# Kernel optimization log

Measured on AMD Instinct MI355X. Metric: run time of the kernel, lower is better.

## Reference

```python
import jax, jax.numpy as jnp
import numpy as np

B, T, NS, NP, F, FO, K1, K2 = 128, 24, 20, 8, 256, 256, 3, 2
ES_EXTRA, EP_EXTRA = 60, 16


def _edges(n, n_extra, seed):
    # ring in both directions guarantees every node has in- and out-degree >= 1
    rng = np.random.default_rng(seed)
    i = np.arange(n)
    src = np.concatenate([i, (i + 1) % n, rng.integers(0, n, n_extra)])
    dst = np.concatenate([(i + 1) % n, i, rng.integers(0, n, n_extra)])
    return jnp.asarray(np.stack([src, dst]).astype(np.int32))


def _dconv(X, row, col, ew, W, b):
    # X: [B, N, Cin], W: [2, K, Cin, Cout]  (torch_geometric_temporal DConv)
    N = X.shape[1]
    deg_out = jnp.zeros((N,), X.dtype).at[row].add(ew)
    deg_in = jnp.zeros((N,), X.dtype).at[col].add(ew)
    norm_out = (1.0 / deg_out)[row]
    norm_in = (1.0 / deg_in)[row]

    def prop(x, norm):
        msg = x[:, row, :] * norm[None, :, None]  # gather at source, scale
        return jnp.zeros_like(x).at[:, col, :].add(msg)  # scatter-add at target

    H = X @ W[0, 0] + X @ W[1, 0]
    K = W.shape[1]
    Tx_0 = X
    if K > 1:
        Tx_1_o = prop(X, norm_out)
        Tx_1_i = prop(X, norm_in)
        H = H + Tx_1_o @ W[0, 1] + Tx_1_i @ W[1, 1]
        for k in range(2, K):
            Tx_2_o = 2.0 * prop(Tx_1_o, norm_out) - Tx_0
            Tx_2_i = 2.0 * prop(Tx_1_i, norm_in) - Tx_0
            H = H + Tx_2_o @ W[0, k] + Tx_2_i @ W[1, k]
            Tx_0, Tx_1_o, Tx_1_i = Tx_1_o, Tx_2_o, Tx_2_i
    return H + b


def _forward(x_dis, x_precip, edge_index_s, edge_weight_s, edge_index_p, edge_weight_p,
             Wz_s, bz_s, Wz_p, bz_p, Wr_s, br_s, Wr_p, br_p, Wh_s, bh_s, Wh_p, bh_p,
             W_ro, b_ro, W_ag, b_ag):
    b_, t_, ns, _ = x_dis.shape
    np_ = x_precip.shape[2]
    fo = Wz_s.shape[-1]
    rs, cs = edge_index_s[0], edge_index_s[1]
    rp, cp = edge_index_p[0], edge_index_p[1]

    def gate(Xs, Xp, Hs, Hp, Ws, bs, Wp, bp):
        Gs = _dconv(jnp.concatenate([Xs, Hs], axis=-1), rs, cs, edge_weight_s, Ws, bs)
        Gp = _dconv(jnp.concatenate([Xp, Hp], axis=-1), rp, cp, edge_weight_p, Wp, bp)
        return jnp.concatenate([Gs, Gp], axis=1)

    def step(H, xt):
        Xs, Xp = xt
        Hs, Hp = H[:, :ns], H[:, ns:]
        Z = jax.nn.sigmoid(gate(Xs, Xp, Hs, Hp, Wz_s, bz_s, Wz_p, bz_p))
        R = jax.nn.sigmoid(gate(Xs, Xp, Hs, Hp, Wr_s, br_s, Wr_p, br_p))
        gH = H * R
        Ht = jnp.tanh(gate(Xs, Xp, gH[:, :ns], gH[:, ns:], Wh_s, bh_s, Wh_p, bh_p))
        return Z * H + (1.0 - Z) * Ht, None

    H0 = jnp.zeros((b_, ns + np_, fo), x_dis.dtype)
    H, _ = jax.lax.scan(step, H0, (jnp.swapaxes(x_dis, 0, 1), jnp.swapaxes(x_precip, 0, 1)))
    out = H @ W_ro + b_ro                       # [B, 28, 1] readout per node
    out = (out[:, :, 0] @ W_ag + b_ag)[:, :, None]  # aggr over 28 nodes -> [B, 5, 1]
    return out


def setup_inputs() -> dict:
    key = jax.random.key(0)
    ks = jax.random.split(key, 24)
    sc = 0.04  # ~1/sqrt(fan_in=512)
    d = {
        'x_dis': jax.random.normal(ks[0], (B, T, NS, F), jnp.float32),
        'x_precip': jax.random.normal(ks[1], (B, T, NP, F), jnp.float32),
        'edge_index_s': _edges(NS, ES_EXTRA, 1),
        'edge_index_p': _edges(NP, EP_EXTRA, 2),
        'edge_weight_s': jax.random.uniform(ks[2], (2 * NS + ES_EXTRA,), jnp.float32, 0.1, 1.0),
        'edge_weight_p': jax.random.uniform(ks[3], (2 * NP + EP_EXTRA,), jnp.float32, 0.1, 1.0),
    }
    names_s = ['Wz_s', 'Wr_s', 'Wh_s']
    names_p = ['Wz_p', 'Wr_p', 'Wh_p']
    for i, n in enumerate(names_s):
        d[n] = sc * jax.random.normal(ks[4 + i], (2, K1, F + FO, FO), jnp.float32)
        d['b' + n[1:]] = sc * jax.random.normal(ks[7 + i], (FO,), jnp.float32)
    for i, n in enumerate(names_p):
        d[n] = sc * jax.random.normal(ks[10 + i], (2, K2, F + FO, FO), jnp.float32)
        d['b' + n[1:]] = sc * jax.random.normal(ks[13 + i], (FO,), jnp.float32)
    d['W_ro'] = sc * jax.random.normal(ks[16], (FO, 1), jnp.float32)
    d['b_ro'] = sc * jax.random.normal(ks[17], (1,), jnp.float32)
    d['W_ag'] = 0.1 * jax.random.normal(ks[18], (NS + NP, 5), jnp.float32)
    d['b_ag'] = 0.1 * jax.random.normal(ks[19], (5,), jnp.float32)
    return d


def reference(x_dis, x_precip, edge_index_s, edge_weight_s, edge_index_p, edge_weight_p,
              Wz_s, bz_s, Wz_p, bz_p, Wr_s, br_s, Wr_p, br_p, Wh_s, bh_s, Wh_p, bh_p,
              W_ro, b_ro, W_ag, b_ag):
    return _forward(x_dis, x_precip, edge_index_s, edge_weight_s, edge_index_p, edge_weight_p,
                    Wz_s, bz_s, Wz_p, bz_p, Wr_s, br_s, Wr_p, br_p, Wh_s, bh_s, Wh_p, bh_p,
                    W_ro, b_ro, W_ag, b_ag)
```

## Files before the change

### kernel.cpp

```cpp
#include <hip/hip_runtime.h>
#include <stdint.h>

#define NSN 20
#define NPN 8
#define NB 128
#define TT 24
#define NN 28
#define ES 100
#define EP 32
#define KHS 1280
#define KHP 768
#define NPRE 768
#define TCH 4

typedef _Float16 half_t;
typedef __attribute__((ext_vector_type(8))) _Float16 f16x8;
typedef __attribute__((ext_vector_type(4))) float f32x4;

__device__ __forceinline__ void gl16(const half_t* g, half_t* l) {
  __builtin_amdgcn_global_load_lds((const __attribute__((address_space(1))) void*)g,
                                   (__attribute__((address_space(3))) void*)l, 16, 0, 0);
}

__global__ void graph_build(const int* __restrict__ ei_s, const float* __restrict__ ew_s,
                            const int* __restrict__ ei_p, const float* __restrict__ ew_p,
                            float* __restrict__ Ms_s, float* __restrict__ Ms_p,
                            float* __restrict__ Mbig_s, float* __restrict__ Mbig_p) {
  __shared__ float Ao[NSN*NSN], Aiw[NSN*NSN], dgo[NSN], dgi[NSN];
  __shared__ float T2o[NSN*NSN], T2i[NSN*NSN];
  __shared__ float Aop[NPN*NPN], Aip[NPN*NPN], dgop[NPN], dgip[NPN];
  int tid = threadIdx.x;
  for (int i = tid; i < NSN*NSN; i += blockDim.x) { Ao[i] = 0.f; Aiw[i] = 0.f; }
  for (int i = tid; i < NPN*NPN; i += blockDim.x) { Aop[i] = 0.f; Aip[i] = 0.f; }
  if (tid < NSN) { dgo[tid] = 0.f; dgi[tid] = 0.f; }
  if (tid < NPN) { dgop[tid] = 0.f; dgip[tid] = 0.f; }
  __syncthreads();
  if (tid == 0) {
    for (int e = 0; e < ES; ++e) { int r = ei_s[e], c = ei_s[ES+e]; float w = ew_s[e]; dgo[r] += w; dgi[c] += w; }
    for (int e = 0; e < ES; ++e) { int r = ei_s[e], c = ei_s[ES+e]; Ao[c*NSN+r] += 1.f/dgo[r]; Aiw[c*NSN+r] += 1.f/dgi[r]; }
  }
  if (tid == 1) {
    for (int e = 0; e < EP; ++e) { int r = ei_p[e], c = ei_p[EP+e]; float w = ew_p[e]; dgop[r] += w; dgip[c] += w; }
    for (int e = 0; e < EP; ++e) { int r = ei_p[e], c = ei_p[EP+e]; Aop[c*NPN+r] += 1.f/dgop[r]; Aip[c*NPN+r] += 1.f/dgip[r]; }
  }
  __syncthreads();
  for (int i = tid; i < NSN*NSN; i += blockDim.x) {
    int r = i / NSN, c = i % NSN;
    float so = 0.f, si = 0.f;
    for (int k = 0; k < NSN; ++k) { so += Ao[r*NSN+k]*Ao[k*NSN+c]; si += Aiw[r*NSN+k]*Aiw[k*NSN+c]; }
    float t2o = 2.f*so - (r==c ? 1.f : 0.f);
    float t2i = 2.f*si - (r==c ? 1.f : 0.f);
    T2o[i] = t2o; T2i[i] = t2i;
    Ms_s[0*NSN*NSN + i] = Ao[i];
    Ms_s[1*NSN*NSN + i] = Aiw[i];
    Ms_s[2*NSN*NSN + i] = t2o;
    Ms_s[3*NSN*NSN + i] = t2i;
  }
  for (int i = tid; i < NPN*NPN; i += blockDim.x) {
    Ms_p[0*NPN*NPN + i] = Aop[i];
    Ms_p[1*NPN*NPN + i] = Aip[i];
  }
  __syncthreads();
  for (int i = tid; i < NSN*NSN*5; i += blockDim.x) {
    int n = i / 100, s = i % 100, r = s / 5, tau = s % 5;
    float v;
    if (tau == 0) v = (n == r) ? 1.f : 0.f;
    else if (tau == 1) v = Ao[n*NSN + r];
    else if (tau == 2) v = Aiw[n*NSN + r];
    else if (tau == 3) v = T2o[n*NSN + r];
    else               v = T2i[n*NSN + r];
    Mbig_s[i] = v;
  }
  for (int i = tid; i < NPN*NPN*3; i += blockDim.x) {
    int n = i / 24, s = i % 24, r = s / 3, tau = s % 3;
    float v;
    if (tau == 0) v = (n == r) ? 1.f : 0.f;
    else if (tau == 1) v = Aop[n*NPN + r];
    else               v = Aip[n*NPN + r];
    Mbig_p[i] = v;
  }
}

__device__ __forceinline__ float wsrc(const float* W, int Kdim, int tau, int i, int jj) {
  if (tau == 0) return W[(size_t)(0*Kdim+0)*512*256 + (size_t)i*256 + jj]
                     + W[(size_t)(1*Kdim+0)*512*256 + (size_t)i*256 + jj];
  int dir = (tau - 1) & 1;
  int k = (tau + 1) >> 1;
  return W[(size_t)(dir*Kdim + k)*512*256 + (size_t)i*256 + jj];
}

__global__ void prep_w(const float* __restrict__ Wz_s, const float* __restrict__ Wr_s, const float* __restrict__ Wh_s,
                       const float* __restrict__ Wz_p, const float* __restrict__ Wr_p, const float* __restrict__ Wh_p,
                       half_t* __restrict__ WX_s, half_t* __restrict__ WX_p,
                       half_t* __restrict__ WHzr_s, half_t* __restrict__ WHh_s,
                       half_t* __restrict__ WHzr_p, half_t* __restrict__ WHh_p) {
  const long c0 = (long)768*KHS;
  const long c1 = c0 + (long)768*KHP;
  const long c2 = c1 + (long)2560*256;
  const long c3 = c2 + (long)1280*256;
  const long c4 = c3 + (long)1536*256;
  const long c5 = c4 + (long)768*256;
  for (long idx = (long)blockIdx.x*256 + threadIdx.x; idx < c5; idx += (long)gridDim.x*256) {
    if (idx < c0) {
      long x = idx; int j = (int)(x / KHS), c = (int)(x % KHS); int tau = c >> 8;
      const float* W = (j < 256) ? Wz_s : (j < 512) ? Wr_s : Wh_s;
      WX_s[x] = (half_t)wsrc(W, 3, tau, c & 255, j & 255);
    } else if (idx < c1) {
      long x = idx - c0; int j = (int)(x / KHP), c = (int)(x % KHP); int tau = c >> 8;
      const float* W = (j < 256) ? Wz_p : (j < 512) ? Wr_p : Wh_p;
      WX_p[x] = (half_t)wsrc(W, 2, tau, c & 255, j & 255);
    } else if (idx < c2) {
      long x = idx - c1; int cc = (int)(x >> 8), f = (int)(x & 255);
      int tau = cc / 512, j = cc % 512;
      const float* W = (j < 256) ? Wz_s : Wr_s;
      WHzr_s[(size_t)cc*256 + f] = (half_t)wsrc(W, 3, tau, 256 + f, j & 255);
    } else if (idx < c3) {
      long x = idx - c2; int cc = (int)(x >> 8), f = (int)(x & 255);
      int tau = cc >> 8, j = cc & 255;
      WHh_s[(size_t)cc*256 + f] = (half_t)wsrc(Wh_s, 3, tau, 256 + f, j);
    } else if (idx < c4) {
      long x = idx - c3; int cc = (int)(x >> 8), f = (int)(x & 255);
      int tau = cc / 512, j = cc % 512;
      const float* W = (j < 256) ? Wz_p : Wr_p;
      WHzr_p[(size_t)cc*256 + f] = (half_t)wsrc(W, 2, tau, 256 + f, j & 255);
    } else {
      long x = idx - c4; int cc = (int)(x >> 8), f = (int)(x & 255);
      int tau = cc >> 8, j = cc & 255;
      WHh_p[(size_t)cc*256 + f] = (half_t)wsrc(Wh_p, 2, tau, 256 + f, j);
    }
  }
}

__global__ void zero_f(float* p, long n) {
  long i = (long)blockIdx.x*256 + threadIdx.x;
  if (i < n) p[i] = 0.f;
}

__global__ __launch_bounds__(256) void chebx(const float* __restrict__ xdis, const float* __restrict__ xpre,
                                             const float* __restrict__ Ms_s, const float* __restrict__ Ms_p,
                                             half_t* __restrict__ XTs, half_t* __restrict__ XTp, int t0) {
  __shared__ float Xc[NSN*256];
  __shared__ float Ml[4*NSN*NSN];
  int bb = blockIdx.x, tid = threadIdx.x;
  bool isP = bb >= NB*TCH;
  int q = isP ? bb - NB*TCH : bb;
  int b = q % NB, tp = q / NB;
  int N = isP ? NPN : NSN, nt = isP ? 3 : 5, KX = nt << 8;
  const float* X = isP ? (xpre + (size_t)(b*TT + t0 + tp)*NPN*256)
                       : (xdis + (size_t)(b*TT + t0 + tp)*NSN*256);
  for (int i = tid; i < N*64; i += 256) ((float4*)Xc)[i] = ((const float4*)X)[i];
  int nm = (nt-1)*N*N;
  const float* Msrc = isP ? Ms_p : Ms_s;
  for (int i = tid; i < nm; i += 256) Ml[i] = Msrc[i];
  __syncthreads();
  half_t* XT = isP ? XTp : XTs;
  size_t rowbase = (size_t)(tp*NB + b)*N;
  int kc8 = KX >> 3, nch = N * kc8;
  for (int i = tid; i < nch; i += 256) {
    int n = i / kc8, c8 = i - n*kc8;
    int tau = c8 >> 5, f0 = (c8 & 31) << 3;
    float v[8];
    if (tau == 0) {
      const float* xr0 = Xc + n*256 + f0;
#pragma unroll
      for (int j = 0; j < 8; ++j) v[j] = xr0[j];
    } else {
      const float* M = Ml + (tau-1)*N*N + n*N;
#pragma unroll
      for (int j = 0; j < 8; ++j) v[j] = 0.f;
      for (int r = 0; r < N; ++r) {
        float m = M[r];
        const float* xr = Xc + r*256 + f0;
#pragma unroll
        for (int j = 0; j < 8; ++j) v[j] += m*xr[j];
      }
    }
    union { uint4 q; half_t u[8]; } hv;
#pragma unroll
    for (int j = 0; j < 8; ++j) hv.u[j] = (half_t)v[j];
    *(uint4*)(XT + (rowbase + n)*(size_t)KX + ((size_t)c8 << 3)) = hv.q;
  }
}

__global__ __launch_bounds__(512) void gemm_pre(
    const half_t* __restrict__ A0, const half_t* __restrict__ B0, int K0,
    int rbS, int cbTot,
    const half_t* __restrict__ A1, const half_t* __restrict__ B1, int K1,
    half_t* __restrict__ Px0, half_t* __restrict__ Px1,
    const float* __restrict__ bz0, const float* __restrict__ br0, const float* __restrict__ bh0,
    const float* __restrict__ bz1, const float* __restrict__ br1, const float* __restrict__ bh1) {
  __shared__ __align__(16) half_t sbuf[3][12288];
  int id = blockIdx.x;
  int xx = id & 7, kq = id >> 3;
  int rbTot8 = (gridDim.x / cbTot) >> 3;
  int rb = xx*rbTot8 + kq / cbTot;
  int cb = kq - (kq / cbTot)*cbTot;

  bool isP = rb >= rbS;
  const half_t* A = isP ? A1 : A0;
  const half_t* B = isP ? B1 : B0;
  int K = isP ? K1 : K0;
  int row0 = (isP ? rb - rbS : rb) * 64;
  int col0 = cb * 128;
  int tid = threadIdx.x, lane = tid & 63, w = tid >> 6;
  int l15 = lane & 15, l4 = lane >> 4;
  int wr = (w >> 2) * 32, wc = (w & 3) * 32;

  const half_t* srcb[3];
  int ldso[3];
#pragma unroll
  for (int j = 0; j < 3; ++j) {
    int c = ((j*8 + w) << 6) + lane;
    const half_t* base;
    if (c < 512) {
      int r = c >> 3, kb = c & 7;
      base = A + (size_t)(row0 + r)*K + ((kb ^ (r & 7)) << 3);
    } else {
      int d = c - 512, r = d >> 3, kb = d & 7;
      base = B + (size_t)(col0 + r)*K + ((kb ^ (r & 7)) << 3);
    }
    srcb[j] = base;
    ldso[j] = c << 3;
  }

  f32x4 acc[2][2];
#pragma unroll
  for (int i = 0; i < 2; ++i)
#pragma unroll
    for (int j = 0; j < 2; ++j) acc[i][j] = (f32x4){0.f,0.f,0.f,0.f};

  int nk = K >> 6;
#define STAGEP(K0E, BUFP)  { half_t* _b = (BUFP); _Pragma("unroll") \
    for (int j = 0; j < 3; ++j) gl16(srcb[j] + (K0E), _b + ldso[j]); }

  STAGEP(0,   &sbuf[0][0]);
  STAGEP(64,  &sbuf[1][0]);
  STAGEP(128, &sbuf[2][0]);

  for (int k = 0; k < nk; ++k) {
    int rem = nk - 1 - k;
    if (rem >= 2)      asm volatile("s_waitcnt vmcnt(6)" ::: "memory");
    else if (rem == 1) asm volatile("s_waitcnt vmcnt(3)" ::: "memory");
    else               asm volatile("s_waitcnt vmcnt(0)" ::: "memory");
    __builtin_amdgcn_s_barrier();
    const half_t* cur = &sbuf[k % 3][0];
    const half_t* cB = cur + 4096;
#pragma unroll
    for (int kk = 0; kk < 2; ++kk) {
      f16x8 af[2], bq[2];
#pragma unroll
      for (int mi = 0; mi < 2; ++mi) {
        int r = wr + mi*16 + l15;
        int sb = (kk*4 + l4) ^ (r & 7);
        af[mi] = *(const f16x8*)&cur[r*64 + sb*8];
      }
#pragma unroll
      for (int ni = 0; ni < 2; ++ni) {
        int r = wc + ni*16 + l15;
        int sb = (kk*4 + l4) ^ (r & 7);
        bq[ni] = *(const f16x8*)&cB[r*64 + sb*8];
      }
#pragma unroll
      for (int mi = 0; mi < 2; ++mi)
#pragma unroll
        for (int ni = 0; ni < 2; ++ni)
          acc[mi][ni] = __builtin_amdgcn_mfma_f32_16x16x32_f16(af[mi], bq[ni], acc[mi][ni], 0, 0, 0);
    }
    __builtin_amdgcn_s_barrier();
    if (k + 3 < nk) STAGEP((k + 3) << 6, &sbuf[k % 3][0]);
  }
#undef STAGEP

  half_t* PxO = isP ? Px1 : Px0;
#pragma unroll
  for (int mi = 0; mi < 2; ++mi)
#pragma unroll
    for (int ni = 0; ni < 2; ++ni) {
      int colg = col0 + wc + ni*16 + l15;
      const float* bias = (colg < 256) ? (isP ? bz1 : bz0)
                        : (colg < 512) ? (isP ? br1 : br0)
                                       : (isP ? bh1 : bh0);
#pragma unroll
      for (int rg = 0; rg < 4; ++rg) {
        int grow = row0 + wr + mi*16 + l4*4 + rg;
        PxO[(size_t)grow*NPRE + colg] = (half_t)(acc[mi][ni][rg] + bias[colg & 255]);
      }
    }
}

__global__ __launch_bounds__(512) void gemm_y(
    const half_t* __restrict__ A0, const half_t* __restrict__ B0, half_t* __restrict__ C0, int NC0, int cb0, int nb0,
    const half_t* __restrict__ A1, const half_t* __restrict__ B1, half_t* __restrict__ C1, int NC1, int cb1) {
  __shared__ __align__(16) half_t sbuf[3][12288];
  int id = blockIdx.x;
  int rb, cb; const half_t *A, *B; half_t* C; int NC;
  if (id < nb0) { rb = id / cb0; cb = id % cb0; A = A0; B = B0; C = C0; NC = NC0; }
  else { int q = id - nb0; rb = q / cb1; cb = q % cb1; A = A1; B = B1; C = C1; NC = NC1; }
  int row0 = rb*64, col0 = cb*128;
  int tid = threadIdx.x, lane = tid & 63, w = tid >> 6;
  int l15 = lane & 15, l4 = lane >> 4;
  int wr = (w >> 2) * 32, wc = (w & 3) * 32;

  const half_t* srcb[3];
  int ldso[3];
#pragma unroll
  for (int j = 0; j < 3; ++j) {
    int c = ((j*8 + w) << 6) + lane;
    const half_t* base;
    if (c < 512) {
      int r = c >> 3, kb = c & 7;
      base = A + (size_t)(row0 + r)*256 + ((kb ^ (r & 7)) << 3);
    } else {
      int d = c - 512, r = d >> 3, kb = d & 7;
      base = B + (size_t)(col0 + r)*256 + ((kb ^ (r & 7)) << 3);
    }
    srcb[j] = base;
    ldso[j] = c << 3;
  }

  f32x4 acc[2][2];
#pragma unroll
  for (int i = 0; i < 2; ++i)
#pragma unroll
    for (int j = 0; j < 2; ++j) acc[i][j] = (f32x4){0.f,0.f,0.f,0.f};

#define STAGEY(K0E, BUFP)  { half_t* _b = (BUFP); _Pragma("unroll") \
    for (int j = 0; j < 3; ++j) gl16(srcb[j] + (K0E), _b + ldso[j]); }

  STAGEY(0,   &sbuf[0][0]);
  STAGEY(64,  &sbuf[1][0]);
  STAGEY(128, &sbuf[2][0]);

  for (int k = 0; k < 4; ++k) {
    int rem = 3 - k;
    if (rem >= 2)      asm volatile("s_waitcnt vmcnt(6)" ::: "memory");
    else if (rem == 1) asm volatile("s_waitcnt vmcnt(3)" ::: "memory");
    else               asm volatile("s_waitcnt vmcnt(0)" ::: "memory");
    __builtin_amdgcn_s_barrier();
    const half_t* cur = &sbuf[k % 3][0];
    const half_t* cB = cur + 4096;
#pragma unroll
    for (int kk = 0; kk < 2; ++kk) {
      f16x8 af[2], bq[2];
#pragma unroll
      for (int mi = 0; mi < 2; ++mi) {
        int r = wr + mi*16 + l15;
        int sb = (kk*4 + l4) ^ (r & 7);
        af[mi] = *(const f16x8*)&cur[r*64 + sb*8];
      }
#pragma unroll
      for (int ni = 0; ni < 2; ++ni) {
        int r = wc + ni*16 + l15;
        int sb = (kk*4 + l4) ^ (r & 7);
        bq[ni] = *(const f16x8*)&cB[r*64 + sb*8];
      }
#pragma unroll
      for (int mi = 0; mi < 2; ++mi)
#pragma unroll
        for (int ni = 0; ni < 2; ++ni)
          acc[mi][ni] = __builtin_amdgcn_mfma_f32_16x16x32_f16(af[mi], bq[ni], acc[mi][ni], 0, 0, 0);
    }
    __builtin_amdgcn_s_barrier();
    if (k + 3 < 4) STAGEY((k + 3) << 6, &sbuf[k % 3][0]);
  }
#undef STAGEY

#pragma unroll
  for (int mi = 0; mi < 2; ++mi)
#pragma unroll
    for (int ni = 0; ni < 2; ++ni) {
      int colg = col0 + wc + ni*16 + l15;
#pragma unroll
      for (int rg = 0; rg < 4; ++rg) {
        int grow = row0 + wr + mi*16 + l4*4 + rg;
        C[(size_t)grow*NC + colg] = (half_t)acc[mi][ni][rg];
      }
    }
}

template<int GATE>
__global__ __launch_bounds__(256) void contract_k(
    const half_t* __restrict__ Ys, const half_t* __restrict__ Yp,
    const half_t* __restrict__ Px_s, const half_t* __restrict__ Px_p,
    const float* __restrict__ Mb_s, const float* __restrict__ Mb_p,
    const float* __restrict__ Hin, float* __restrict__ Z,
    half_t* __restrict__ Out_s, half_t* __restrict__ Out_p,
    float* __restrict__ Hout) {
  constexpr int JB = GATE ? 2 : 4;
  constexpr int JW = GATE ? 256 : 512;
  __shared__ float Yl[100*128];
  __shared__ float Mb[NSN*100];
  int id = blockIdx.x, tid = threadIdx.x;
  bool isP = id >= NB*JB;
  int q = isP ? id - NB*JB : id;
  int b = q / JB, jb = q % JB;
  int N = isP ? NPN : NSN, ntau = isP ? 3 : 5;
  int nseg = N * ntau;
  int NC = ntau * JW;
  const half_t* Y = isP ? Yp : Ys;
  const float* Mbg = isP ? Mb_p : Mb_s;
  int tot8 = nseg << 4;
  for (int i = tid; i < tot8; i += 256) {
    int seg = i >> 4, q8 = i & 15;
    int r = seg / ntau, tau = seg - r*ntau;
    union { uint4 qq; half_t u[8]; } uu;
    uu.qq = *(const uint4*)&Y[(size_t)(b*N + r)*NC + tau*JW + jb*128 + (q8 << 3)];
    float* dst = Yl + (seg << 7) + (q8 << 3);
#pragma unroll
    for (int e = 0; e < 8; ++e) dst[e] = (float)uu.u[e];
  }
  for (int i = tid; i < N*nseg; i += 256) Mb[i] = Mbg[i];
  __syncthreads();
  f32x4* Yl4 = (f32x4*)Yl;
  const half_t* Px = isP ? Px_p : Px_s;
  half_t* Out = isP ? Out_p : Out_s;
  int hoff = isP ? NSN : 0;
  int nout4 = N << 5;
  for (int o = tid; o < nout4; o += 256) {
    int n = o >> 5, j4 = o & 31;
    int j = jb*128 + (j4 << 2);
    f32x4 p = (f32x4){0.f,0.f,0.f,0.f};
    const float* mrow = Mb + n*nseg;
    for (int s = 0; s < nseg; ++s) {
      float m = mrow[s];
      f32x4 y = Yl4[(s << 5) + j4];
      p += m*y;
    }
    union { uint2 qq; half_t u[4]; } pu;
    pu.qq = *(const uint2*)&Px[(size_t)(b*N + n)*NPRE + (GATE ? 512 : 0) + j];
#pragma unroll
    for (int e = 0; e < 4; ++e) p[e] += (float)pu.u[e];
    if constexpr (GATE == 0) {
      if (j < 256) {
        f32x4 sg;
#pragma unroll
        for (int e = 0; e < 4; ++e) sg[e] = 1.f/(1.f + expf(-p[e]));
        *(f32x4*)&Z[((size_t)b*NN + hoff + n)*256 + j] = sg;
      } else {
        int f = j - 256;
        f32x4 h = *(const f32x4*)&Hin[((size_t)b*NN + hoff + n)*256 + f];
        union { uint2 qq; half_t u[4]; } ho;
#pragma unroll
        for (int e = 0; e < 4; ++e) ho.u[e] = (half_t)(h[e]/(1.f + expf(-p[e])));
        *(uint2*)(Out + (size_t)(b*N + n)*256 + f) = ho.qq;
      }
    } else {
      size_t hidx = ((size_t)b*NN + hoff + n)*256 + j;
      f32x4 zv = *(const f32x4*)&Z[hidx];
      f32x4 hv = *(const f32x4*)&Hin[hidx];
      f32x4 hn;
      union { uint2 qq; half_t u[4]; } ho;
#pragma unroll
      for (int e = 0; e < 4; ++e) {
        float ht = tanhf(p[e]);
        hn[e] = zv[e]*hv[e] + (1.f - zv[e])*ht;
        ho.u[e] = (half_t)hn[e];
      }
      *(f32x4*)&Hout[hidx] = hn;
      *(uint2*)(Out + (size_t)(b*N + n)*256 + j) = ho.qq;
    }
  }
}

__global__ __launch_bounds__(256) void readout_k(const float* __restrict__ H, const float* __restrict__ W_ro,
                                                 const float* __restrict__ b_ro, const float* __restrict__ W_ag,
                                                 const float* __restrict__ b_ag, float* __restrict__ out) {
  __shared__ float red[256];
  __shared__ float o1[NN];
  int b = blockIdx.x, tid = threadIdx.x;
  float wro = W_ro[tid];
  for (int n = 0; n < NN; ++n) {
    red[tid] = H[((size_t)b*NN + n)*256 + tid] * wro;
    __syncthreads();
    for (int s = 128; s > 0; s >>= 1) { if (tid < s) red[tid] += red[tid+s]; __syncthreads(); }
    if (tid == 0) o1[n] = red[0] + b_ro[0];
    __syncthreads();
  }
  if (tid < 5) {
    float s = b_ag[tid];
    for (int n = 0; n < NN; ++n) s += o1[n] * W_ag[n*5 + tid];
    out[b*5 + tid] = s;
  }
}

extern "C" void kernel_launch(void* const* d_in, const int* in_sizes, int n_in,
                              void* d_out, int out_size, void* d_ws, size_t ws_size,
                              hipStream_t stream) {
  const float* xdis = (const float*)d_in[0];
  const float* xpre = (const float*)d_in[1];
  const int*   ei_s = (const int*)d_in[2];
  const int*   ei_p = (const int*)d_in[3];
  const float* ew_s = (const float*)d_in[4];
  const float* ew_p = (const float*)d_in[5];
  const float* Wz_s = (const float*)d_in[6];
  const float* bz_s = (const float*)d_in[7];
  const float* Wr_s = (const float*)d_in[8];
  const float* br_s = (const float*)d_in[9];
  const float* Wh_s = (const float*)d_in[10];
  const float* bh_s = (const float*)d_in[11];
  const float* Wz_p = (const float*)d_in[12];
  const float* bz_p = (const float*)d_in[13];
  const float* Wr_p = (const float*)d_in[14];
  const float* br_p = (const float*)d_in[15];
  const float* Wh_p = (const float*)d_in[16];
  const float* bh_p = (const float*)d_in[17];
  const float* W_ro = (const float*)d_in[18];
  const float* b_ro = (const float*)d_in[19];
  const float* W_ag = (const float*)d_in[20];
  const float* b_ag = (const float*)d_in[21];
  float* out = (float*)d_out;
  (void)in_sizes; (void)n_in; (void)out_size; (void)ws_size;

  char* w = (char*)d_ws;
  size_t off = 0;
  auto alloc = [&](size_t bytes) { void* p = w + off; off = (off + bytes + 255) & ~(size_t)255; return p; };

  const size_t rowsXs = (size_t)TCH*NB*NSN, rowsXp = (size_t)TCH*NB*NPN;

  float* Ms_s = (float*)alloc(4*NSN*NSN*sizeof(float));
  float* Ms_p = (float*)alloc(2*NPN*NPN*sizeof(float));
  float* Mbig_s = (float*)alloc(NSN*100*sizeof(float));
  float* Mbig_p = (float*)alloc(NPN*24*sizeof(float));
  half_t* WX_s = (half_t*)alloc((size_t)768*KHS*2);
  half_t* WX_p = (half_t*)alloc((size_t)768*KHP*2);
  half_t* WHzr_s = (half_t*)alloc((size_t)2560*256*2);
  half_t* WHh_s  = (half_t*)alloc((size_t)1280*256*2);
  half_t* WHzr_p = (half_t*)alloc((size_t)1536*256*2);
  half_t* WHh_p  = (half_t*)alloc((size_t)768*256*2);
  half_t* XT_s = (half_t*)alloc(rowsXs*KHS*2);
  half_t* XT_p = (half_t*)alloc(rowsXp*KHP*2);
  half_t* Px_s = (half_t*)alloc((size_t)TT*NB*NSN*NPRE*2);
  half_t* Px_p = (half_t*)alloc((size_t)TT*NB*NPN*NPRE*2);
  half_t* Y_s = (half_t*)alloc((size_t)NB*NSN*2560*2);
  half_t* Y_p = (half_t*)alloc((size_t)NB*NPN*1536*2);
  float* H  = (float*)alloc((size_t)NB*NN*256*4);
  float* Z  = (float*)alloc((size_t)NB*NN*256*4);
  half_t* Hf  = (half_t*)alloc((size_t)NB*NN*256*2);
  half_t* gHf = (half_t*)alloc((size_t)NB*NN*256*2);
  half_t* Hf_s = Hf,  * Hf_p = Hf + (size_t)NB*NSN*256;
  half_t* gHf_s = gHf, * gHf_p = gHf + (size_t)NB*NSN*256;

  graph_build<<<1, 64, 0, stream>>>(ei_s, ew_s, ei_p, ew_p, Ms_s, Ms_p, Mbig_s, Mbig_p);
  prep_w<<<1024, 256, 0, stream>>>(Wz_s, Wr_s, Wh_s, Wz_p, Wr_p, Wh_p,
                                   WX_s, WX_p, WHzr_s, WHh_s, WHzr_p, WHh_p);
  const long nH = (long)NB*NN*256;
  zero_f<<<(nH + 255)/256, 256, 0, stream>>>(H, nH);
  zero_f<<<(nH/2 + 255)/256, 256, 0, stream>>>((float*)Hf, nH/2);

  for (int t0 = 0; t0 < TT; t0 += TCH) {
    chebx<<<2*NB*TCH, 256, 0, stream>>>(xdis, xpre, Ms_s, Ms_p, XT_s, XT_p, t0);
    gemm_pre<<<224*6, 512, 0, stream>>>(
        XT_s, WX_s, KHS, 160, 6,
        XT_p, WX_p, KHP,
        Px_s + (size_t)t0*NB*NSN*NPRE, Px_p + (size_t)t0*NB*NPN*NPRE,
        bz_s, br_s, bh_s, bz_p, br_p, bh_p);
  }

  for (int t = 0; t < TT; ++t) {
    const half_t* PxS = Px_s + (size_t)t*NB*NSN*NPRE;
    const half_t* PxP = Px_p + (size_t)t*NB*NPN*NPRE;
    gemm_y<<<800 + 192, 512, 0, stream>>>(Hf_s, WHzr_s, Y_s, 2560, 20, 800,
                                          Hf_p, WHzr_p, Y_p, 1536, 12);
    contract_k<0><<<NB*4*2, 256, 0, stream>>>(Y_s, Y_p, PxS, PxP, Mbig_s, Mbig_p,
                                              H, Z, gHf_s, gHf_p, nullptr);
    gemm_y<<<400 + 96, 512, 0, stream>>>(gHf_s, WHh_s, Y_s, 1280, 10, 400,
                                         gHf_p, WHh_p, Y_p, 768, 6);
    contract_k<1><<<NB*2*2, 256, 0, stream>>>(Y_s, Y_p, PxS, PxP, Mbig_s, Mbig_p,
                                              H, Z, Hf_s, Hf_p, H);
  }
  readout_k<<<NB, 256, 0, stream>>>(H, W_ro, b_ro, W_ag, b_ag, out);
}
```

Baseline: 1.693 ms.

## Fuse recurrent hidden-state GEMM with graph contraction into one per-step kernel

```diff
diff --git a/kernel.cpp b/kernel.cpp
--- a/kernel.cpp
+++ b/kernel.cpp
@@ -29,19 +29,25 @@
   __shared__ float Ao[NSN*NSN], Aiw[NSN*NSN], dgo[NSN], dgi[NSN];
   __shared__ float T2o[NSN*NSN], T2i[NSN*NSN];
   __shared__ float Aop[NPN*NPN], Aip[NPN*NPN], dgop[NPN], dgip[NPN];
+  __shared__ int eis[2*ES]; __shared__ float ews[ES];
+  __shared__ int eip[2*EP]; __shared__ float ewp[EP];
   int tid = threadIdx.x;
+  for (int i = tid; i < 2*ES; i += blockDim.x) eis[i] = ei_s[i];
+  for (int i = tid; i < ES; i += blockDim.x) ews[i] = ew_s[i];
+  for (int i = tid; i < 2*EP; i += blockDim.x) eip[i] = ei_p[i];
+  for (int i = tid; i < EP; i += blockDim.x) ewp[i] = ew_p[i];
   for (int i = tid; i < NSN*NSN; i += blockDim.x) { Ao[i] = 0.f; Aiw[i] = 0.f; }
   for (int i = tid; i < NPN*NPN; i += blockDim.x) { Aop[i] = 0.f; Aip[i] = 0.f; }
   if (tid < NSN) { dgo[tid] = 0.f; dgi[tid] = 0.f; }
   if (tid < NPN) { dgop[tid] = 0.f; dgip[tid] = 0.f; }
   __syncthreads();
   if (tid == 0) {
-    for (int e = 0; e < ES; ++e) { int r = ei_s[e], c = ei_s[ES+e]; float w = ew_s[e]; dgo[r] += w; dgi[c] += w; }
-    for (int e = 0; e < ES; ++e) { int r = ei_s[e], c = ei_s[ES+e]; Ao[c*NSN+r] += 1.f/dgo[r]; Aiw[c*NSN+r] += 1.f/dgi[r]; }
+    for (int e = 0; e < ES; ++e) { int r = eis[e], c = eis[ES+e]; float w = ews[e]; dgo[r] += w; dgi[c] += w; }
+    for (int e = 0; e < ES; ++e) { int r = eis[e], c = eis[ES+e]; Ao[c*NSN+r] += 1.f/dgo[r]; Aiw[c*NSN+r] += 1.f/dgi[r]; }
   }
   if (tid == 1) {
-    for (int e = 0; e < EP; ++e) { int r = ei_p[e], c = ei_p[EP+e]; float w = ew_p[e]; dgop[r] += w; dgip[c] += w; }
-    for (int e = 0; e < EP; ++e) { int r = ei_p[e], c = ei_p[EP+e]; Aop[c*NPN+r] += 1.f/dgop[r]; Aip[c*NPN+r] += 1.f/dgip[r]; }
+    for (int e = 0; e < EP; ++e) { int r = eip[e], c = eip[EP+e]; float w = ewp[e]; dgop[r] += w; dgip[c] += w; }
+    for (int e = 0; e < EP; ++e) { int r = eip[e], c = eip[EP+e]; Aop[c*NPN+r] += 1.f/dgop[r]; Aip[c*NPN+r] += 1.f/dgip[r]; }
   }
   __syncthreads();
   for (int i = tid; i < NSN*NSN; i += blockDim.x) {
@@ -288,176 +294,201 @@
     }
 }
 
-__global__ __launch_bounds__(512) void gemm_y(
-    const half_t* __restrict__ A0, const half_t* __restrict__ B0, half_t* __restrict__ C0, int NC0, int cb0, int nb0,
-    const half_t* __restrict__ A1, const half_t* __restrict__ B1, half_t* __restrict__ C1, int NC1, int cb1) {
-  __shared__ __align__(16) half_t sbuf[3][12288];
-  int id = blockIdx.x;
-  int rb, cb; const half_t *A, *B; half_t* C; int NC;
-  if (id < nb0) { rb = id / cb0; cb = id % cb0; A = A0; B = B0; C = C0; NC = NC0; }
-  else { int q = id - nb0; rb = q / cb1; cb = q % cb1; A = A1; B = B1; C = C1; NC = NC1; }
-  int row0 = rb*64, col0 = cb*128;
-  int tid = threadIdx.x, lane = tid & 63, w = tid >> 6;
-  int l15 = lane & 15, l4 = lane >> 4;
-  int wr = (w >> 2) * 32, wc = (w & 3) * 32;
-
-  const half_t* srcb[3];
-  int ldso[3];
-#pragma unroll
-  for (int j = 0; j < 3; ++j) {
-    int c = ((j*8 + w) << 6) + lane;
-    const half_t* base;
-    if (c < 512) {
-      int r = c >> 3, kb = c & 7;
-      base = A + (size_t)(row0 + r)*256 + ((kb ^ (r & 7)) << 3);
-    } else {
-      int d = c - 512, r = d >> 3, kb = d & 7;
-      base = B + (size_t)(col0 + r)*256 + ((kb ^ (r & 7)) << 3);
-    }
-    srcb[j] = base;
-    ldso[j] = c << 3;
-  }
-
-  f32x4 acc[2][2];
-#pragma unroll
-  for (int i = 0; i < 2; ++i)
-#pragma unroll
-    for (int j = 0; j < 2; ++j) acc[i][j] = (f32x4){0.f,0.f,0.f,0.f};
-
-#define STAGEY(K0E, BUFP)  { half_t* _b = (BUFP); _Pragma("unroll") \
-    for (int j = 0; j < 3; ++j) gl16(srcb[j] + (K0E), _b + ldso[j]); }
-
-  STAGEY(0,   &sbuf[0][0]);
-  STAGEY(64,  &sbuf[1][0]);
-  STAGEY(128, &sbuf[2][0]);
-
-  for (int k = 0; k < 4; ++k) {
-    int rem = 3 - k;
-    if (rem >= 2)      asm volatile("s_waitcnt vmcnt(6)" ::: "memory");
-    else if (rem == 1) asm volatile("s_waitcnt vmcnt(3)" ::: "memory");
-    else               asm volatile("s_waitcnt vmcnt(0)" ::: "memory");
-    __builtin_amdgcn_s_barrier();
-    const half_t* cur = &sbuf[k % 3][0];
-    const half_t* cB = cur + 4096;
-#pragma unroll
-    for (int kk = 0; kk < 2; ++kk) {
-      f16x8 af[2], bq[2];
-#pragma unroll
-      for (int mi = 0; mi < 2; ++mi) {
-        int r = wr + mi*16 + l15;
-        int sb = (kk*4 + l4) ^ (r & 7);
-        af[mi] = *(const f16x8*)&cur[r*64 + sb*8];
-      }
-#pragma unroll
-      for (int ni = 0; ni < 2; ++ni) {
-        int r = wc + ni*16 + l15;
-        int sb = (kk*4 + l4) ^ (r & 7);
-        bq[ni] = *(const f16x8*)&cB[r*64 + sb*8];
-      }
-#pragma unroll
-      for (int mi = 0; mi < 2; ++mi)
-#pragma unroll
-        for (int ni = 0; ni < 2; ++ni)
-          acc[mi][ni] = __builtin_amdgcn_mfma_f32_16x16x32_f16(af[mi], bq[ni], acc[mi][ni], 0, 0, 0);
-    }
-    __builtin_amdgcn_s_barrier();
-    if (k + 3 < 4) STAGEY((k + 3) << 6, &sbuf[k % 3][0]);
-  }
-#undef STAGEY
-
-#pragma unroll
-  for (int mi = 0; mi < 2; ++mi)
-#pragma unroll
-    for (int ni = 0; ni < 2; ++ni) {
-      int colg = col0 + wc + ni*16 + l15;
-#pragma unroll
-      for (int rg = 0; rg < 4; ++rg) {
-        int grow = row0 + wr + mi*16 + l4*4 + rg;
-        C[(size_t)grow*NC + colg] = (half_t)acc[mi][ni][rg];
-      }
-    }
-}
-
 template<int GATE>
-__global__ __launch_bounds__(256) void contract_k(
-    const half_t* __restrict__ Ys, const half_t* __restrict__ Yp,
+__global__ __launch_bounds__(512) void rec_k(
+    const half_t* __restrict__ Asrc_s, const half_t* __restrict__ Asrc_p,
+    const half_t* __restrict__ WH_s, const half_t* __restrict__ WH_p,
     const half_t* __restrict__ Px_s, const half_t* __restrict__ Px_p,
     const float* __restrict__ Mb_s, const float* __restrict__ Mb_p,
     const float* __restrict__ Hin, float* __restrict__ Z,
     half_t* __restrict__ Out_s, half_t* __restrict__ Out_p,
-    float* __restrict__ Hout) {
+    float* __restrict__ Hout, int nSblk) {
   constexpr int JB = GATE ? 2 : 4;
   constexpr int JW = GATE ? 256 : 512;
-  __shared__ float Yl[100*128];
-  __shared__ float Mb[NSN*100];
+  __shared__ __align__(16) half_t ring[2][20480];
+  __shared__ __align__(16) half_t Hl[32*264];
+  __shared__ float Mbl[2000];
+  half_t* Yt = &ring[0][0];
+
   int id = blockIdx.x, tid = threadIdx.x;
-  bool isP = id >= NB*JB;
-  int q = isP ? id - NB*JB : id;
-  int b = q / JB, jb = q % JB;
-  int N = isP ? NPN : NSN, ntau = isP ? 3 : 5;
-  int nseg = N * ntau;
-  int NC = ntau * JW;
-  const half_t* Y = isP ? Yp : Ys;
-  const float* Mbg = isP ? Mb_p : Mb_s;
-  int tot8 = nseg << 4;
-  for (int i = tid; i < tot8; i += 256) {
-    int seg = i >> 4, q8 = i & 15;
-    int r = seg / ntau, tau = seg - r*ntau;
-    union { uint4 qq; half_t u[8]; } uu;
-    uu.qq = *(const uint4*)&Y[(size_t)(b*N + r)*NC + tau*JW + jb*128 + (q8 << 3)];
-    float* dst = Yl + (seg << 7) + (q8 << 3);
-#pragma unroll
-    for (int e = 0; e < 8; ++e) dst[e] = (float)uu.u[e];
-  }
-  for (int i = tid; i < N*nseg; i += 256) Mb[i] = Mbg[i];
+  int lane = tid & 63, w = tid >> 6;
+  int l15 = lane & 15, l4 = lane >> 4;
+  bool isP = id >= nSblk;
+  int q = isP ? id - nSblk : id;
+  int bb = q / JB, jb = q - bb*JB;
+  int NTAU = isP ? 3 : 5;
+  int NCOL = NTAU << 7;
+  int NW = NTAU << 4;
+  int nld = NTAU;
+  const half_t* B = isP ? WH_p : WH_s;
+
+  if (!isP) {
+    const half_t* src = Asrc_s + (size_t)bb*20*256;
+    for (int c = tid; c < 640; c += 512) {
+      int r = c >> 5, qq = c & 31;
+      *(uint4*)&Hl[r*264 + qq*8] = *(const uint4*)&src[(size_t)r*256 + qq*8];
+    }
+    for (int i = tid; i < 2000; i += 512) Mbl[i] = Mb_s[i];
+  } else {
+    const half_t* src = Asrc_p + (size_t)bb*32*256;
+    for (int c = tid; c < 1024; c += 512) {
+      int r = c >> 5, qq = c & 31;
+      *(uint4*)&Hl[r*264 + qq*8] = *(const uint4*)&src[(size_t)r*256 + qq*8];
+    }
+    for (int i = tid; i < 192; i += 512) Mbl[i] = Mb_p[i];
+  }
+
+  const half_t* bsrc[5];
+  int bdst[5];
+#pragma unroll
+  for (int j = 0; j < 5; ++j) {
+    int c = j*512 + tid;
+    int r = c >> 2, kb = c & 3;
+    int jc = r / NTAU, tau = r - jc*NTAU;
+    int gcol = tau*JW + (jb << 7) + jc;
+    bsrc[j] = B + (size_t)gcol*256 + ((kb ^ (r & 3)) << 3);
+    bdst[j] = c << 3;
+  }
+
+  int ab[2];
+#pragma unroll
+  for (int mi = 0; mi < 2; ++mi) {
+    int row = mi*16 + l15;
+    int hr = isP ? row : (row < 20 ? row : 19);
+    ab[mi] = hr*264 + l4*8;
+  }
+  int bboff[5];
+#pragma unroll
+  for (int ni = 0; ni < 5; ++ni) {
+    int col = w*NW + ni*16 + l15;
+    int cc = (ni < nld) ? col : 0;
+    bboff[ni] = cc*32 + ((l4 ^ (cc & 3)) << 3);
+  }
+
+  f32x4 acc[2][5];
+#pragma unroll
+  for (int i = 0; i < 2; ++i)
+#pragma unroll
+    for (int j = 0; j < 5; ++j) acc[i][j] = (f32x4){0.f,0.f,0.f,0.f};
+
+#define BSTAGE(K0E, BUFP) { half_t* _b = (BUFP); _Pragma("unroll") \
+    for (int j = 0; j < 5; ++j) if (j < nld) gl16(bsrc[j] + (K0E), _b + bdst[j]); }
+
+  BSTAGE(0, &ring[0][0]);
   __syncthreads();
-  f32x4* Yl4 = (f32x4*)Yl;
+
+  for (int k = 0; k < 8; ++k) {
+    if (k < 7) {
+      BSTAGE((k + 1) << 5, &ring[(k + 1) & 1][0]);
+      if (!isP) asm volatile("s_waitcnt vmcnt(5)" ::: "memory");
+      else      asm volatile("s_waitcnt vmcnt(3)" ::: "memory");
+    } else {
+      asm volatile("s_waitcnt vmcnt(0)" ::: "memory");
+    }
+    __builtin_amdgcn_s_barrier();
+    const half_t* cur = &ring[k & 1][0];
+    f16x8 af[2], bq[5];
+#pragma unroll
+    for (int mi = 0; mi < 2; ++mi) af[mi] = *(const f16x8*)&Hl[ab[mi] + (k << 5)];
+#pragma unroll
+    for (int ni = 0; ni < 5; ++ni) if (ni < nld) bq[ni] = *(const f16x8*)&cur[bboff[ni]];
+#pragma unroll
+    for (int mi = 0; mi < 2; ++mi)
+#pragma unroll
+      for (int ni = 0; ni < 5; ++ni) if (ni < nld)
+        acc[mi][ni] = __builtin_amdgcn_mfma_f32_16x16x32_f16(af[mi], bq[ni], acc[mi][ni], 0, 0, 0);
+    __builtin_amdgcn_s_barrier();
+  }
+#undef BSTAGE
+
+#pragma unroll
+  for (int ni = 0; ni < 5; ++ni) if (ni < nld) {
+    int col = w*NW + ni*16 + l15;
+    int jc = col / NTAU, tau = col - jc*NTAU;
+#pragma unroll
+    for (int mi = 0; mi < 2; ++mi) {
+#pragma unroll
+      for (int rg = 0; rg < 4; ++rg) {
+        int r = mi*16 + l4*4 + rg;
+        if (!isP) {
+          if (r < 20) Yt[jc*100 + r*5 + tau] = (half_t)acc[mi][ni][rg];
+        } else {
+          Yt[jc*100 + (r >> 3)*24 + (r & 7)*3 + tau] = (half_t)acc[mi][ni][rg];
+        }
+      }
+    }
+  }
+  __syncthreads();
+
   const half_t* Px = isP ? Px_p : Px_s;
-  half_t* Out = isP ? Out_p : Out_s;
-  int hoff = isP ? NSN : 0;
-  int nout4 = N << 5;
-  for (int o = tid; o < nout4; o += 256) {
-    int n = o >> 5, j4 = o & 31;
-    int j = jb*128 + (j4 << 2);
-    f32x4 p = (f32x4){0.f,0.f,0.f,0.f};
-    const float* mrow = Mb + n*nseg;
-    for (int s = 0; s < nseg; ++s) {
-      float m = mrow[s];
-      f32x4 y = Yl4[(s << 5) + j4];
-      p += m*y;
-    }
-    union { uint2 qq; half_t u[4]; } pu;
-    pu.qq = *(const uint2*)&Px[(size_t)(b*N + n)*NPRE + (GATE ? 512 : 0) + j];
-#pragma unroll
-    for (int e = 0; e < 4; ++e) p[e] += (float)pu.u[e];
-    if constexpr (GATE == 0) {
-      if (j < 256) {
-        f32x4 sg;
-#pragma unroll
-        for (int e = 0; e < 4; ++e) sg[e] = 1.f/(1.f + expf(-p[e]));
-        *(f32x4*)&Z[((size_t)b*NN + hoff + n)*256 + j] = sg;
+  constexpr int PXOFF = GATE ? 512 : 0;
+  if (!isP) {
+    int b = bb;
+    for (int o = tid; o < 20*128; o += 512) {
+      int n = o >> 7, jc = o & 127;
+      const float* mr = Mbl + n*100;
+      const half_t* yc = Yt + jc*100;
+      float p = 0.f;
+#pragma unroll
+      for (int g = 0; g < 25; ++g) {
+        union { uint2 qv; half_t u[4]; } yy;
+        yy.qv = *(const uint2*)&yc[g*4];
+#pragma unroll
+        for (int e = 0; e < 4; ++e) p += mr[g*4 + e]*(float)yy.u[e];
+      }
+      int colg = (jb << 7) + jc;
+      p += (float)Px[((size_t)b*20 + n)*NPRE + PXOFF + colg];
+      size_t hrow = (size_t)b*NN + n;
+      if constexpr (GATE == 0) {
+        if (jb < 2) {
+          Z[hrow*256 + colg] = 1.f/(1.f + expf(-p));
+        } else {
+          int f = colg - 256;
+          float gh = Hin[hrow*256 + f]/(1.f + expf(-p));
+          Out_s[((size_t)b*20 + n)*256 + f] = (half_t)gh;
+        }
       } else {
-        int f = j - 256;
-        f32x4 h = *(const f32x4*)&Hin[((size_t)b*NN + hoff + n)*256 + f];
-        union { uint2 qq; half_t u[4]; } ho;
-#pragma unroll
-        for (int e = 0; e < 4; ++e) ho.u[e] = (half_t)(h[e]/(1.f + expf(-p[e])));
-        *(uint2*)(Out + (size_t)(b*N + n)*256 + f) = ho.qq;
-      }
-    } else {
-      size_t hidx = ((size_t)b*NN + hoff + n)*256 + j;
-      f32x4 zv = *(const f32x4*)&Z[hidx];
-      f32x4 hv = *(const f32x4*)&Hin[hidx];
-      f32x4 hn;
-      union { uint2 qq; half_t u[4]; } ho;
-#pragma unroll
-      for (int e = 0; e < 4; ++e) {
-        float ht = tanhf(p[e]);
-        hn[e] = zv[e]*hv[e] + (1.f - zv[e])*ht;
-        ho.u[e] = (half_t)hn[e];
-      }
-      *(f32x4*)&Hout[hidx] = hn;
-      *(uint2*)(Out + (size_t)(b*N + n)*256 + j) = ho.qq;
+        size_t hidx = hrow*256 + colg;
+        float ht = tanhf(p);
+        float z = Z[hidx];
+        float hn = z*Hin[hidx] + (1.f - z)*ht;
+        Hout[hidx] = hn;
+        Out_s[((size_t)b*20 + n)*256 + colg] = (half_t)hn;
+      }
+    }
+  } else {
+    for (int o = tid; o < 4*8*128; o += 512) {
+      int bq = o >> 10, n = (o >> 7) & 7, jc = o & 127;
+      int b = bb*4 + bq;
+      const float* mr = Mbl + n*24;
+      const half_t* yc = Yt + jc*100 + bq*24;
+      float p = 0.f;
+#pragma unroll
+      for (int g = 0; g < 6; ++g) {
+        union { uint2 qv; half_t u[4]; } yy;
+        yy.qv = *(const uint2*)&yc[g*4];
+#pragma unroll
+        for (int e = 0; e < 4; ++e) p += mr[g*4 + e]*(float)yy.u[e];
+      }
+      int colg = (jb << 7) + jc;
+      p += (float)Px[((size_t)b*8 + n)*NPRE + PXOFF + colg];
+      size_t hrow = (size_t)b*NN + NSN + n;
+      if constexpr (GATE == 0) {
+        if (jb < 2) {
+          Z[hrow*256 + colg] = 1.f/(1.f + expf(-p));
+        } else {
+          int f = colg - 256;
+          float gh = Hin[hrow*256 + f]/(1.f + expf(-p));
+          Out_p[((size_t)b*8 + n)*256 + f] = (half_t)gh;
+        }
+      } else {
+        size_t hidx = hrow*256 + colg;
+        float ht = tanhf(p);
+        float z = Z[hidx];
+        float hn = z*Hin[hidx] + (1.f - z)*ht;
+        Hout[hidx] = hn;
+        Out_p[((size_t)b*8 + n)*256 + colg] = (half_t)hn;
+      }
     }
   }
 }
@@ -531,8 +562,6 @@
   half_t* XT_p = (half_t*)alloc(rowsXp*KHP*2);
   half_t* Px_s = (half_t*)alloc((size_t)TT*NB*NSN*NPRE*2);
   half_t* Px_p = (half_t*)alloc((size_t)TT*NB*NPN*NPRE*2);
-  half_t* Y_s = (half_t*)alloc((size_t)NB*NSN*2560*2);
-  half_t* Y_p = (half_t*)alloc((size_t)NB*NPN*1536*2);
   float* H  = (float*)alloc((size_t)NB*NN*256*4);
   float* Z  = (float*)alloc((size_t)NB*NN*256*4);
   half_t* Hf  = (half_t*)alloc((size_t)NB*NN*256*2);
@@ -559,14 +588,12 @@
   for (int t = 0; t < TT; ++t) {
     const half_t* PxS = Px_s + (size_t)t*NB*NSN*NPRE;
     const half_t* PxP = Px_p + (size_t)t*NB*NPN*NPRE;
-    gemm_y<<<800 + 192, 512, 0, stream>>>(Hf_s, WHzr_s, Y_s, 2560, 20, 800,
-                                          Hf_p, WHzr_p, Y_p, 1536, 12);
-    contract_k<0><<<NB*4*2, 256, 0, stream>>>(Y_s, Y_p, PxS, PxP, Mbig_s, Mbig_p,
-                                              H, Z, gHf_s, gHf_p, nullptr);
-    gemm_y<<<400 + 96, 512, 0, stream>>>(gHf_s, WHh_s, Y_s, 1280, 10, 400,
-                                         gHf_p, WHh_p, Y_p, 768, 6);
-    contract_k<1><<<NB*2*2, 256, 0, stream>>>(Y_s, Y_p, PxS, PxP, Mbig_s, Mbig_p,
-                                              H, Z, Hf_s, Hf_p, H);
+    rec_k<0><<<NB*4 + 32*4, 512, 0, stream>>>(
+        Hf_s, Hf_p, WHzr_s, WHzr_p, PxS, PxP, Mbig_s, Mbig_p,
+        H, Z, gHf_s, gHf_p, nullptr, NB*4);
+    rec_k<1><<<NB*2 + 32*2, 512, 0, stream>>>(
+        gHf_s, gHf_p, WHh_s, WHh_p, PxS, PxP, Mbig_s, Mbig_p,
+        H, Z, Hf_s, Hf_p, H, NB*2);
   }
   readout_k<<<NB, 256, 0, stream>>>(H, W_ro, b_ro, W_ag, b_ag, out);
 }
```

Result: slower. 2.320 ms (+37.0%).
